# Performance work log

Hardware: AMD Instinct MI355X
Metric: run time of the kernel (lower is better)

Reference implementation:

```python
import jax, jax.numpy as jnp
import numpy as np

B, L, H, P, A, T = 64, 256, 1024, 64, 512, 8


def setup_inputs() -> dict:
    key = jax.random.key(0)
    ks = jax.random.split(key, 9)
    return {
        "word_hiddens": jax.random.normal(ks[0], (B, L, H), dtype=jnp.float32),
        "pos_e1_embeddings": jax.random.normal(ks[1], (B, L, P), dtype=jnp.float32),
        "pos_e2_embeddings": jax.random.normal(ks[2], (B, L, P), dtype=jnp.float32),
        "e1_end": jax.random.randint(ks[3], (B,), 0, L, dtype=jnp.int32),
        "e2_end": jax.random.randint(ks[4], (B,), 0, L, dtype=jnp.int32),
        "type_embeddings": jax.random.normal(ks[5], (T, H), dtype=jnp.float32) * 0.03,
        "W_pos": jax.random.normal(ks[6], (H + 2 * P, A), dtype=jnp.float32) * 0.03,
        "W_ent": jax.random.normal(ks[7], (4 * H, A), dtype=jnp.float32) * 0.02,
        "v": jax.random.normal(ks[8], (A,), dtype=jnp.float32) * 0.05,
    }


def _latent_type(e_h, type_emb):
    # alpha = softmax(e_h @ C^T); latent type = alpha @ C   (C: [T, latent])
    scores = jnp.einsum("bh,th->bt", e_h, type_emb)
    alpha = jax.nn.softmax(scores, axis=-1)
    return jnp.einsum("bt,th->bh", alpha, type_emb)


def reference(word_hiddens, pos_e1_embeddings, pos_e2_embeddings, e1_end, e2_end,
              type_embeddings, W_pos, W_ent, v):
    b, seq_len, h = word_hiddens.shape
    batch_idx = jnp.arange(b)
    e1_h = word_hiddens[batch_idx, e1_end]          # [B, H]
    e2_h = word_hiddens[batch_idx, e2_end]          # [B, H]
    e1_type = _latent_type(e1_h, type_embeddings)   # [B, H]
    e2_type = _latent_type(e2_h, type_embeddings)   # [B, H]

    entity_features = jnp.concatenate([e1_h, e1_type, e2_h, e2_type], axis=-1)  # [B, 4H]
    pos_features = jnp.concatenate([word_hiddens, pos_e1_embeddings, pos_e2_embeddings], axis=-1)  # [B, L, H+2P]

    dense_pos = jnp.einsum("blf,fa->bla", pos_features, W_pos)   # [B, L, A]
    dense_ent = entity_features @ W_ent                          # [B, A]
    # Faithful to original tf.repeat(axis=1)+reshape (element-interleaved, not a broadcast)
    dense_ent_r = jnp.repeat(dense_ent, seq_len, axis=1).reshape(b, seq_len, -1)  # [B, L, A]

    u = jnp.tanh(dense_pos + dense_ent_r)            # [B, L, A]
    vu = jnp.einsum("bla,a->bl", u, v)               # [B, L]
    alpha = jax.nn.softmax(vu, axis=-1)              # [B, L]
    z = jnp.einsum("blh,bl->bh", word_hiddens, alpha)  # [B, H]
    return z
```

## Files before the change

kernel.cpp:

```cpp
#include <hip/hip_runtime.h>
#include <hip/hip_bf16.h>
#include <math.h>

#define B_ 64
#define L_ 256
#define H_ 1024
#define P_ 64
#define A_ 512
#define T_ 8
#define KDIM 1152
#define NSTEP 36

typedef __attribute__((ext_vector_type(8))) __bf16 bf16x8;
typedef __attribute__((ext_vector_type(4))) float f32x4;

__device__ __forceinline__ float bf2f(ushort u) {
  union { unsigned int i; float f; } v; v.i = ((unsigned int)u) << 16; return v.f;
}
__device__ __forceinline__ ushort f2bf_rne(float f) {
  union { float f; unsigned int i; } v; v.f = f;
  unsigned int r = v.i + 0x7FFFu + ((v.i >> 16) & 1u);
  return (ushort)(r >> 16);
}
__device__ __forceinline__ unsigned int pack2_rne(float a, float b) {
  return (unsigned int)f2bf_rne(a) | ((unsigned int)f2bf_rne(b) << 16);
}

template <bool BF16>
__device__ __forceinline__ float ld1(const void* p, size_t i) {
  if (BF16) return bf2f(((const ushort*)p)[i]);
  return ((const float*)p)[i];
}
template <bool BF16>
__device__ __forceinline__ float4 ld4(const void* p, size_t i) {
  if (BF16) {
    ushort4 u = *(const ushort4*)((const ushort*)p + i);
    return (float4){bf2f(u.x), bf2f(u.y), bf2f(u.z), bf2f(u.w)};
  }
  return *(const float4*)((const float*)p + i);
}

__global__ __launch_bounds__(256) void detect_dtype(const ushort* __restrict__ wh,
                                                    int* __restrict__ flag) {
  __shared__ int cnt;
  if (threadIdx.x == 0) cnt = 0;
  __syncthreads();
  int c = 0;
  for (int i = threadIdx.x; i < 8192; i += 256) {
    int e = (wh[i] >> 7) & 0xFF;
    if (e >= 110 && e <= 135) c++;
  }
  atomicAdd(&cnt, c);
  __syncthreads();
  if (threadIdx.x == 0) flag[0] = (cnt > 6553) ? 1 : 0;
}

template <bool BF16>
__global__ __launch_bounds__(256) void build_wts(const void* __restrict__ W,
                                                 ushort* __restrict__ WTs,
                                                 const int* __restrict__ flag) {
  if ((*flag != 0) != BF16) return;
  __shared__ ushort tile[32][33];
  const int s  = blockIdx.x >> 4;
  const int at = blockIdx.x & 15;
  const int tx = threadIdx.x & 31;
  const int ty = threadIdx.x >> 5;
#pragma unroll
  for (int i = 0; i < 4; ++i) {
    size_t idx = (size_t)(s * 32 + ty + i * 8) * A_ + at * 32 + tx;
    ushort u;
    if (BF16) u = ((const ushort*)W)[idx];
    else u = f2bf_rne(((const float*)W)[idx]);
    tile[ty + i * 8][tx] = u;
  }
  __syncthreads();
#pragma unroll
  for (int i = 0; i < 4; ++i) {
    WTs[(size_t)s * (A_ * 32) + (size_t)(at * 32 + ty + i * 8) * 32 + tx] =
        tile[tx][ty + i * 8];
  }
}

template <bool BF16>
__global__ __launch_bounds__(256) void entity_features_k(
    const void* __restrict__ wh, const int* __restrict__ e1e,
    const int* __restrict__ e2e, const void* __restrict__ temb,
    float* __restrict__ EF, const int* __restrict__ flag) {
  if ((*flag != 0) != BF16) return;
  const int b = blockIdx.x;
  const int tid = threadIdx.x;
  __shared__ float eh1[1024];
  __shared__ float eh2[1024];
  __shared__ float part[256][16];
  __shared__ float scores[16];
  __shared__ float alpha[16];

  const size_t o1 = ((size_t)b * L_ + e1e[b]) * H_;
  const size_t o2 = ((size_t)b * L_ + e2e[b]) * H_;
  for (int h = tid; h < 1024; h += 256) {
    eh1[h] = ld1<BF16>(wh, o1 + h);
    eh2[h] = ld1<BF16>(wh, o2 + h);
  }
  __syncthreads();

  float p[16];
#pragma unroll
  for (int t = 0; t < 16; ++t) p[t] = 0.f;
  for (int h = tid; h < 1024; h += 256) {
    float a1 = eh1[h], a2 = eh2[h];
#pragma unroll
    for (int t = 0; t < 8; ++t) {
      float c = ld1<BF16>(temb, t * 1024 + h);
      p[t] += a1 * c;
      p[8 + t] += a2 * c;
    }
  }
#pragma unroll
  for (int t = 0; t < 16; ++t) part[tid][t] = p[t];
  __syncthreads();
  if (tid < 16) {
    float s = 0.f;
    for (int i = 0; i < 256; ++i) s += part[i][tid];
    scores[tid] = s;
  }
  __syncthreads();
  if (tid < 2) {
    const int base = tid * 8;
    float mx = scores[base];
    for (int t = 1; t < 8; ++t) mx = fmaxf(mx, scores[base + t]);
    float sum = 0.f;
    float e[8];
    for (int t = 0; t < 8; ++t) { e[t] = __expf(scores[base + t] - mx); sum += e[t]; }
    float inv = 1.f / sum;
    for (int t = 0; t < 8; ++t) alpha[base + t] = e[t] * inv;
  }
  __syncthreads();

  float* efb = EF + (size_t)b * 4096;
  for (int h = tid; h < 1024; h += 256) {
    float l1 = 0.f, l2 = 0.f;
#pragma unroll
    for (int t = 0; t < 8; ++t) {
      float c = ld1<BF16>(temb, t * 1024 + h);
      l1 += alpha[t] * c;
      l2 += alpha[8 + t] * c;
    }
    efb[h] = eh1[h];
    efb[1024 + h] = l1;
    efb[2048 + h] = eh2[h];
    efb[3072 + h] = l2;
  }
}

template <bool BF16>
__global__ __launch_bounds__(256) void ent_gemm(const float* __restrict__ EF,
                                                const void* __restrict__ went,
                                                float* __restrict__ part,
                                                const int* __restrict__ flag) {
  if ((*flag != 0) != BF16) return;
  const int nb = blockIdx.x & 3;
  const int kb = blockIdx.x >> 2;
  const int tid = threadIdx.x;
  __shared__ float efs[64][128];

  const int k0 = kb * 128;
  {
    const int kq = (tid & 31) * 4;
    for (int m = tid >> 5; m < 64; m += 8) {
      *(float4*)&efs[m][kq] = *(const float4*)&EF[(size_t)m * 4096 + k0 + kq];
    }
  }
  __syncthreads();

  const int n0 = nb * 128 + (tid & 31) * 4;
  const int mg = (tid >> 5) * 8;
  float acc[8][4];
#pragma unroll
  for (int i = 0; i < 8; ++i)
#pragma unroll
    for (int j = 0; j < 4; ++j) acc[i][j] = 0.f;

  for (int k = 0; k < 128; ++k) {
    float4 w = ld4<BF16>(went, (size_t)(k0 + k) * A_ + n0);
#pragma unroll
    for (int i = 0; i < 8; ++i) {
      float e = efs[mg + i][k];
      acc[i][0] += e * w.x;
      acc[i][1] += e * w.y;
      acc[i][2] += e * w.z;
      acc[i][3] += e * w.w;
    }
  }
#pragma unroll
  for (int i = 0; i < 8; ++i) {
    *(float4*)&part[((size_t)kb * 64 + mg + i) * A_ + n0] =
        (float4){acc[i][0], acc[i][1], acc[i][2], acc[i][3]};
  }
}

__global__ __launch_bounds__(256) void ent_reduce(const float* __restrict__ part,
                                                  float* __restrict__ dense_ent) {
  const int idx = blockIdx.x * 256 + threadIdx.x;
  float s = 0.f;
#pragma unroll
  for (int kb = 0; kb < 32; ++kb) s += part[(size_t)kb * 32768 + idx];
  dense_ent[idx] = s;
}

template <bool BF16>
__global__ __launch_bounds__(256) void fused_gemm_vu(
    const void* __restrict__ wh, const void* __restrict__ pe1,
    const void* __restrict__ pe2, const ushort* __restrict__ WTs,
    const float* __restrict__ dense_ent, const void* __restrict__ vvec,
    float* __restrict__ vu_part, const int* __restrict__ flag) {
  if ((*flag != 0) != BF16) return;
  __shared__ __align__(16) ushort Abuf[2][64 * 40];
  __shared__ __align__(16) ushort Bbuf[2][256 * 40];
  __shared__ float vu_s[4][64];

  const int tid = threadIdx.x;
  const int nb = blockIdx.x & 1;
  const int mb = blockIdx.x >> 1;
  const int rbase = mb * 64;
  const int wave = tid >> 6;
  const int lane = tid & 63;
  const int quad = lane >> 4;
  const int col = lane & 15;

  const int arow = tid >> 2;
  const int akq = (tid & 3) * 8;
  const int myrow = rbase + arow;
  const ushort* bbase = WTs + (size_t)nb * (256 * 32) + (size_t)tid * 32;

  f32x4 acc[4][4];
#pragma unroll
  for (int i = 0; i < 4; ++i)
#pragma unroll
    for (int j = 0; j < 4; ++j) acc[i][j] = (f32x4){0.f, 0.f, 0.f, 0.f};

  uint4 aR, bR0, bR1;

  {
    const size_t off = (size_t)myrow * H_ + 0 * 32 + akq;
    if (BF16) {
      aR = *(const uint4*)((const ushort*)wh + off);
    } else {
      float4 f0 = *(const float4*)((const float*)wh + off);
      float4 f1 = *(const float4*)((const float*)wh + off + 4);
      aR.x = pack2_rne(f0.x, f0.y); aR.y = pack2_rne(f0.z, f0.w);
      aR.z = pack2_rne(f1.x, f1.y); aR.w = pack2_rne(f1.z, f1.w);
    }
    const ushort* bs = bbase;
    bR0 = *(const uint4*)(bs + 0);
    bR1 = *(const uint4*)(bs + 8);
  }
  uint4 bR2 = *(const uint4*)(bbase + 16);
  uint4 bR3 = *(const uint4*)(bbase + 24);
  {
    *(uint4*)&Abuf[0][arow * 40 + akq] = aR;
    ushort* bd = &Bbuf[0][tid * 40];
    *(uint4*)(bd + 0)  = bR0;
    *(uint4*)(bd + 8)  = bR1;
    *(uint4*)(bd + 16) = bR2;
    *(uint4*)(bd + 24) = bR3;
  }
  __syncthreads();

  for (int s = 0; s < NSTEP; ++s) {
    const int cur = s & 1;

    if (s < NSTEP - 1) {
      const int sn = s + 1;
      const void* srcA;
      int ldA, k0A;
      if (sn < 32)      { srcA = wh;  ldA = H_; k0A = sn * 32; }
      else if (sn < 34) { srcA = pe1; ldA = P_; k0A = (sn - 32) * 32; }
      else              { srcA = pe2; ldA = P_; k0A = (sn - 34) * 32; }
      const size_t off = (size_t)myrow * ldA + k0A + akq;
      if (BF16) {
        aR = *(const uint4*)((const ushort*)srcA + off);
      } else {
        float4 f0 = *(const float4*)((const float*)srcA + off);
        float4 f1 = *(const float4*)((const float*)srcA + off + 4);
        aR.x = pack2_rne(f0.x, f0.y); aR.y = pack2_rne(f0.z, f0.w);
        aR.z = pack2_rne(f1.x, f1.y); aR.w = pack2_rne(f1.z, f1.w);
      }
      const ushort* bs = bbase + (size_t)sn * (A_ * 32);
      bR0 = *(const uint4*)(bs + 0);
      bR1 = *(const uint4*)(bs + 8);
      bR2 = *(const uint4*)(bs + 16);
      bR3 = *(const uint4*)(bs + 24);
    }

    bf16x8 af[4], bfr[4];
#pragma unroll
    for (int mf = 0; mf < 4; ++mf)
      af[mf] = *(const bf16x8*)&Abuf[cur][(mf * 16 + col) * 40 + quad * 8];
#pragma unroll
    for (int nf = 0; nf < 4; ++nf)
      bfr[nf] = *(const bf16x8*)&Bbuf[cur][(wave * 64 + nf * 16 + col) * 40 + quad * 8];
#pragma unroll
    for (int mf = 0; mf < 4; ++mf)
#pragma unroll
      for (int nf = 0; nf < 4; ++nf)
        acc[mf][nf] = __builtin_amdgcn_mfma_f32_16x16x32_bf16(af[mf], bfr[nf], acc[mf][nf], 0, 0, 0);

    if (s < NSTEP - 1) {
      const int nxt = cur ^ 1;
      *(uint4*)&Abuf[nxt][arow * 40 + akq] = aR;
      ushort* bd = &Bbuf[nxt][tid * 40];
      *(uint4*)(bd + 0)  = bR0;
      *(uint4*)(bd + 8)  = bR1;
      *(uint4*)(bd + 16) = bR2;
      *(uint4*)(bd + 24) = bR3;
      __syncthreads();
    }
  }

  float vv[4];
#pragma unroll
  for (int nf = 0; nf < 4; ++nf)
    vv[nf] = ld1<BF16>(vvec, nb * 256 + wave * 64 + nf * 16 + col);

#pragma unroll
  for (int mf = 0; mf < 4; ++mf) {
    const int row0 = mf * 16 + quad * 4;
    const int r0 = rbase + row0;
    const int bidx = r0 >> 8;
    const int l0 = r0 & 255;
    const float* ebase = dense_ent + bidx * A_ + 2 * l0 + nb;
    float e0 = ebase[0], e1 = ebase[2], e2 = ebase[4], e3 = ebase[6];
    float s0 = 0.f, s1 = 0.f, s2 = 0.f, s3 = 0.f;
#pragma unroll
    for (int nf = 0; nf < 4; ++nf) {
      float vn = vv[nf];
      s0 += tanhf(acc[mf][nf][0] + e0) * vn;
      s1 += tanhf(acc[mf][nf][1] + e1) * vn;
      s2 += tanhf(acc[mf][nf][2] + e2) * vn;
      s3 += tanhf(acc[mf][nf][3] + e3) * vn;
    }
    s0 += __shfl_xor(s0, 1); s0 += __shfl_xor(s0, 2); s0 += __shfl_xor(s0, 4); s0 += __shfl_xor(s0, 8);
    s1 += __shfl_xor(s1, 1); s1 += __shfl_xor(s1, 2); s1 += __shfl_xor(s1, 4); s1 += __shfl_xor(s1, 8);
    s2 += __shfl_xor(s2, 1); s2 += __shfl_xor(s2, 2); s2 += __shfl_xor(s2, 4); s2 += __shfl_xor(s2, 8);
    s3 += __shfl_xor(s3, 1); s3 += __shfl_xor(s3, 2); s3 += __shfl_xor(s3, 4); s3 += __shfl_xor(s3, 8);
    if (col == 0) {
      vu_s[wave][row0 + 0] = s0;
      vu_s[wave][row0 + 1] = s1;
      vu_s[wave][row0 + 2] = s2;
      vu_s[wave][row0 + 3] = s3;
    }
  }
  __syncthreads();
  if (tid < 64) {
    float s = vu_s[0][tid] + vu_s[1][tid] + vu_s[2][tid] + vu_s[3][tid];
    vu_part[(size_t)nb * (B_ * L_) + rbase + tid] = s;
  }
}

template <bool BF16>
__global__ __launch_bounds__(256) void softmax_z(const void* __restrict__ wh,
                                                 const float* __restrict__ vu_part,
                                                 void* __restrict__ out,
                                                 const int* __restrict__ flag) {
  if ((*flag != 0) != BF16) return;
  const int b = blockIdx.x >> 2;
  const int hq = blockIdx.x & 3;
  const int tid = threadIdx.x;
  __shared__ float alpha[256];
  __shared__ float red[256];

  float x = vu_part[b * L_ + tid] + vu_part[B_ * L_ + b * L_ + tid];
  red[tid] = x;
  __syncthreads();
  for (int s = 128; s > 0; s >>= 1) {
    if (tid < s) red[tid] = fmaxf(red[tid], red[tid + s]);
    __syncthreads();
  }
  float m = red[0];
  __syncthreads();
  float e = __expf(x - m);
  red[tid] = e;
  __syncthreads();
  for (int s = 128; s > 0; s >>= 1) {
    if (tid < s) red[tid] += red[tid + s];
    __syncthreads();
  }
  alpha[tid] = e / red[0];
  __syncthreads();

  const int h = hq * 256 + tid;
  const size_t base = (size_t)b * L_ * H_ + h;
  float a0 = 0.f, a1 = 0.f, a2 = 0.f, a3 = 0.f;
  for (int l = 0; l < 256; l += 4) {
    a0 += alpha[l + 0] * ld1<BF16>(wh, base + (size_t)(l + 0) * H_);
    a1 += alpha[l + 1] * ld1<BF16>(wh, base + (size_t)(l + 1) * H_);
    a2 += alpha[l + 2] * ld1<BF16>(wh, base + (size_t)(l + 2) * H_);
    a3 += alpha[l + 3] * ld1<BF16>(wh, base + (size_t)(l + 3) * H_);
  }
  float z = (a0 + a1) + (a2 + a3);
  if (BF16) ((ushort*)out)[b * H_ + h] = f2bf_rne(z);
  else ((float*)out)[b * H_ + h] = z;
}

extern "C" void kernel_launch(void* const* d_in, const int* in_sizes, int n_in,
                              void* d_out, int out_size, void* d_ws, size_t ws_size,
                              hipStream_t stream) {
  const void* wh   = d_in[0];
  const void* pe1  = d_in[1];
  const void* pe2  = d_in[2];
  const int*  e1e  = (const int*)d_in[3];
  const int*  e2e  = (const int*)d_in[4];
  const void* temb = d_in[5];
  const void* wpos = d_in[6];
  const void* went = d_in[7];
  const void* vvec = d_in[8];

  char* ws = (char*)d_ws;
  int*   flag      = (int*)ws;
  ushort* WTs      = (ushort*)(ws + 256);
  float* dense_ent = (float*)(ws + 1179904);
  float* vu_part   = (float*)(ws + 1310976);
  float* EF        = (float*)(ws + 1442048);
  float* part      = (float*)(ws + 2490624);

  detect_dtype<<<dim3(1), dim3(256), 0, stream>>>((const ushort*)wh, flag);

  build_wts<true ><<<dim3(576), dim3(256), 0, stream>>>(wpos, WTs, flag);
  build_wts<false><<<dim3(576), dim3(256), 0, stream>>>(wpos, WTs, flag);

  entity_features_k<true ><<<dim3(64), dim3(256), 0, stream>>>(wh, e1e, e2e, temb, EF, flag);
  entity_features_k<false><<<dim3(64), dim3(256), 0, stream>>>(wh, e1e, e2e, temb, EF, flag);

  ent_gemm<true ><<<dim3(128), dim3(256), 0, stream>>>(EF, went, part, flag);
  ent_gemm<false><<<dim3(128), dim3(256), 0, stream>>>(EF, went, part, flag);

  ent_reduce<<<dim3(128), dim3(256), 0, stream>>>(part, dense_ent);

  fused_gemm_vu<true ><<<dim3(512), dim3(256), 0, stream>>>(wh, pe1, pe2, WTs, dense_ent, vvec, vu_part, flag);
  fused_gemm_vu<false><<<dim3(512), dim3(256), 0, stream>>>(wh, pe1, pe2, WTs, dense_ent, vvec, vu_part, flag);

  softmax_z<true ><<<dim3(256), dim3(256), 0, stream>>>(wh, vu_part, d_out, flag);
  softmax_z<false><<<dim3(256), dim3(256), 0, stream>>>(wh, vu_part, d_out, flag);
}
```

Measured before the change: 217.1 us.

## Pick dtype on host, retile fused GEMM to 4 N-blocks, split entity GEMM

Removes the on-device dtype detection kernel and the paired bf16/fp32 launches guarded by a flag. The dtype is now chosen on the host from the input byte size, so only one launch runs per stage. The fused position GEMM now uses 128-column N tiles across 4 N-blocks with a 2x2 wave layout, giving 1024 blocks. The entity GEMM is split over M halves, giving 256 blocks. The softmax-weighted sum is unrolled to 8 accumulators, and the workspace is repacked so EF and vu_part share memory. This aims to cut launch overhead and improve occupancy, at the cost of extra B-tile reloads, more partial vu sums, and relying on in_sizes to infer the dtype.

```diff
diff --git a/kernel.cpp b/kernel.cpp
--- a/kernel.cpp
+++ b/kernel.cpp
@@ -40,26 +40,9 @@
   return *(const float4*)((const float*)p + i);
 }
 
-__global__ __launch_bounds__(256) void detect_dtype(const ushort* __restrict__ wh,
-                                                    int* __restrict__ flag) {
-  __shared__ int cnt;
-  if (threadIdx.x == 0) cnt = 0;
-  __syncthreads();
-  int c = 0;
-  for (int i = threadIdx.x; i < 8192; i += 256) {
-    int e = (wh[i] >> 7) & 0xFF;
-    if (e >= 110 && e <= 135) c++;
-  }
-  atomicAdd(&cnt, c);
-  __syncthreads();
-  if (threadIdx.x == 0) flag[0] = (cnt > 6553) ? 1 : 0;
-}
-
 template <bool BF16>
 __global__ __launch_bounds__(256) void build_wts(const void* __restrict__ W,
-                                                 ushort* __restrict__ WTs,
-                                                 const int* __restrict__ flag) {
-  if ((*flag != 0) != BF16) return;
+                                                 ushort* __restrict__ WTs) {
   __shared__ ushort tile[32][33];
   const int s  = blockIdx.x >> 4;
   const int at = blockIdx.x & 15;
@@ -85,8 +68,7 @@
 __global__ __launch_bounds__(256) void entity_features_k(
     const void* __restrict__ wh, const int* __restrict__ e1e,
     const int* __restrict__ e2e, const void* __restrict__ temb,
-    float* __restrict__ EF, const int* __restrict__ flag) {
-  if ((*flag != 0) != BF16) return;
+    float* __restrict__ EF) {
   const int b = blockIdx.x;
   const int tid = threadIdx.x;
   __shared__ float eh1[1024];
@@ -155,35 +137,34 @@
 template <bool BF16>
 __global__ __launch_bounds__(256) void ent_gemm(const float* __restrict__ EF,
                                                 const void* __restrict__ went,
-                                                float* __restrict__ part,
-                                                const int* __restrict__ flag) {
-  if ((*flag != 0) != BF16) return;
-  const int nb = blockIdx.x & 3;
-  const int kb = blockIdx.x >> 2;
+                                                float* __restrict__ part) {
+  const int mh = blockIdx.x & 1;
+  const int nb = (blockIdx.x >> 1) & 3;
+  const int kb = blockIdx.x >> 3;
   const int tid = threadIdx.x;
-  __shared__ float efs[64][128];
+  __shared__ float efs[32][128];
 
   const int k0 = kb * 128;
   {
     const int kq = (tid & 31) * 4;
-    for (int m = tid >> 5; m < 64; m += 8) {
-      *(float4*)&efs[m][kq] = *(const float4*)&EF[(size_t)m * 4096 + k0 + kq];
+    for (int m = tid >> 5; m < 32; m += 8) {
+      *(float4*)&efs[m][kq] = *(const float4*)&EF[(size_t)(mh * 32 + m) * 4096 + k0 + kq];
     }
   }
   __syncthreads();
 
   const int n0 = nb * 128 + (tid & 31) * 4;
-  const int mg = (tid >> 5) * 8;
-  float acc[8][4];
-#pragma unroll
-  for (int i = 0; i < 8; ++i)
+  const int mg = (tid >> 5) * 4;
+  float acc[4][4];
+#pragma unroll
+  for (int i = 0; i < 4; ++i)
 #pragma unroll
     for (int j = 0; j < 4; ++j) acc[i][j] = 0.f;
 
   for (int k = 0; k < 128; ++k) {
     float4 w = ld4<BF16>(went, (size_t)(k0 + k) * A_ + n0);
 #pragma unroll
-    for (int i = 0; i < 8; ++i) {
+    for (int i = 0; i < 4; ++i) {
       float e = efs[mg + i][k];
       acc[i][0] += e * w.x;
       acc[i][1] += e * w.y;
@@ -192,8 +173,8 @@
     }
   }
 #pragma unroll
-  for (int i = 0; i < 8; ++i) {
-    *(float4*)&part[((size_t)kb * 64 + mg + i) * A_ + n0] =
+  for (int i = 0; i < 4; ++i) {
+    *(float4*)&part[((size_t)kb * 64 + mh * 32 + mg + i) * A_ + n0] =
         (float4){acc[i][0], acc[i][1], acc[i][2], acc[i][3]};
   }
 }
@@ -212,36 +193,39 @@
     const void* __restrict__ wh, const void* __restrict__ pe1,
     const void* __restrict__ pe2, const ushort* __restrict__ WTs,
     const float* __restrict__ dense_ent, const void* __restrict__ vvec,
-    float* __restrict__ vu_part, const int* __restrict__ flag) {
-  if ((*flag != 0) != BF16) return;
+    float* __restrict__ vu_part) {
   __shared__ __align__(16) ushort Abuf[2][64 * 40];
-  __shared__ __align__(16) ushort Bbuf[2][256 * 40];
+  __shared__ __align__(16) ushort Bbuf[2][128 * 40];
   __shared__ float vu_s[4][64];
 
   const int tid = threadIdx.x;
-  const int nb = blockIdx.x & 1;
-  const int mb = blockIdx.x >> 1;
+  const int nb = blockIdx.x & 3;
+  const int mb = blockIdx.x >> 2;
   const int rbase = mb * 64;
   const int wave = tid >> 6;
   const int lane = tid & 63;
   const int quad = lane >> 4;
   const int col = lane & 15;
+  const int wr = wave >> 1;
+  const int wc = wave & 1;
 
   const int arow = tid >> 2;
   const int akq = (tid & 3) * 8;
   const int myrow = rbase + arow;
-  const ushort* bbase = WTs + (size_t)nb * (256 * 32) + (size_t)tid * 32;
-
-  f32x4 acc[4][4];
-#pragma unroll
-  for (int i = 0; i < 4; ++i)
+  const int brow = tid >> 1;
+  const int bk0 = (tid & 1) * 16;
+  const ushort* bbase = WTs + (size_t)(nb * 128 + brow) * 32 + bk0;
+
+  f32x4 acc[2][4];
+#pragma unroll
+  for (int i = 0; i < 2; ++i)
 #pragma unroll
     for (int j = 0; j < 4; ++j) acc[i][j] = (f32x4){0.f, 0.f, 0.f, 0.f};
 
   uint4 aR, bR0, bR1;
 
   {
-    const size_t off = (size_t)myrow * H_ + 0 * 32 + akq;
+    const size_t off = (size_t)myrow * H_ + akq;
     if (BF16) {
       aR = *(const uint4*)((const ushort*)wh + off);
     } else {
@@ -250,19 +234,14 @@
       aR.x = pack2_rne(f0.x, f0.y); aR.y = pack2_rne(f0.z, f0.w);
       aR.z = pack2_rne(f1.x, f1.y); aR.w = pack2_rne(f1.z, f1.w);
     }
-    const ushort* bs = bbase;
-    bR0 = *(const uint4*)(bs + 0);
-    bR1 = *(const uint4*)(bs + 8);
-  }
-  uint4 bR2 = *(const uint4*)(bbase + 16);
-  uint4 bR3 = *(const uint4*)(bbase + 24);
+    bR0 = *(const uint4*)(bbase + 0);
+    bR1 = *(const uint4*)(bbase + 8);
+  }
   {
     *(uint4*)&Abuf[0][arow * 40 + akq] = aR;
-    ushort* bd = &Bbuf[0][tid * 40];
-    *(uint4*)(bd + 0)  = bR0;
-    *(uint4*)(bd + 8)  = bR1;
-    *(uint4*)(bd + 16) = bR2;
-    *(uint4*)(bd + 24) = bR3;
+    ushort* bd = &Bbuf[0][brow * 40 + bk0];
+    *(uint4*)(bd + 0) = bR0;
+    *(uint4*)(bd + 8) = bR1;
   }
   __syncthreads();
 
@@ -288,19 +267,17 @@
       const ushort* bs = bbase + (size_t)sn * (A_ * 32);
       bR0 = *(const uint4*)(bs + 0);
       bR1 = *(const uint4*)(bs + 8);
-      bR2 = *(const uint4*)(bs + 16);
-      bR3 = *(const uint4*)(bs + 24);
-    }
-
-    bf16x8 af[4], bfr[4];
-#pragma unroll
-    for (int mf = 0; mf < 4; ++mf)
-      af[mf] = *(const bf16x8*)&Abuf[cur][(mf * 16 + col) * 40 + quad * 8];
+    }
+
+    bf16x8 af[2], bfr[4];
+#pragma unroll
+    for (int mf = 0; mf < 2; ++mf)
+      af[mf] = *(const bf16x8*)&Abuf[cur][(wr * 32 + mf * 16 + col) * 40 + quad * 8];
 #pragma unroll
     for (int nf = 0; nf < 4; ++nf)
-      bfr[nf] = *(const bf16x8*)&Bbuf[cur][(wave * 64 + nf * 16 + col) * 40 + quad * 8];
-#pragma unroll
-    for (int mf = 0; mf < 4; ++mf)
+      bfr[nf] = *(const bf16x8*)&Bbuf[cur][(wc * 64 + nf * 16 + col) * 40 + quad * 8];
+#pragma unroll
+    for (int mf = 0; mf < 2; ++mf)
 #pragma unroll
       for (int nf = 0; nf < 4; ++nf)
         acc[mf][nf] = __builtin_amdgcn_mfma_f32_16x16x32_bf16(af[mf], bfr[nf], acc[mf][nf], 0, 0, 0);
@@ -308,11 +285,9 @@
     if (s < NSTEP - 1) {
       const int nxt = cur ^ 1;
       *(uint4*)&Abuf[nxt][arow * 40 + akq] = aR;
-      ushort* bd = &Bbuf[nxt][tid * 40];
-      *(uint4*)(bd + 0)  = bR0;
-      *(uint4*)(bd + 8)  = bR1;
-      *(uint4*)(bd + 16) = bR2;
-      *(uint4*)(bd + 24) = bR3;
+      ushort* bd = &Bbuf[nxt][brow * 40 + bk0];
+      *(uint4*)(bd + 0) = bR0;
+      *(uint4*)(bd + 8) = bR1;
       __syncthreads();
     }
   }
@@ -320,15 +295,15 @@
   float vv[4];
 #pragma unroll
   for (int nf = 0; nf < 4; ++nf)
-    vv[nf] = ld1<BF16>(vvec, nb * 256 + wave * 64 + nf * 16 + col);
-
-#pragma unroll
-  for (int mf = 0; mf < 4; ++mf) {
-    const int row0 = mf * 16 + quad * 4;
+    vv[nf] = ld1<BF16>(vvec, nb * 128 + wc * 64 + nf * 16 + col);
+
+#pragma unroll
+  for (int mf = 0; mf < 2; ++mf) {
+    const int row0 = wr * 32 + mf * 16 + quad * 4;
     const int r0 = rbase + row0;
     const int bidx = r0 >> 8;
     const int l0 = r0 & 255;
-    const float* ebase = dense_ent + bidx * A_ + 2 * l0 + nb;
+    const float* ebase = dense_ent + bidx * A_ + 2 * l0 + (nb >> 1);
     float e0 = ebase[0], e1 = ebase[2], e2 = ebase[4], e3 = ebase[6];
     float s0 = 0.f, s1 = 0.f, s2 = 0.f, s3 = 0.f;
 #pragma unroll
@@ -352,7 +327,8 @@
   }
   __syncthreads();
   if (tid < 64) {
-    float s = vu_s[0][tid] + vu_s[1][tid] + vu_s[2][tid] + vu_s[3][tid];
+    const int wrr = tid >> 5;
+    float s = vu_s[wrr * 2][tid] + vu_s[wrr * 2 + 1][tid];
     vu_part[(size_t)nb * (B_ * L_) + rbase + tid] = s;
   }
 }
@@ -360,16 +336,16 @@
 template <bool BF16>
 __global__ __launch_bounds__(256) void softmax_z(const void* __restrict__ wh,
                                                  const float* __restrict__ vu_part,
-                                                 void* __restrict__ out,
-                                                 const int* __restrict__ flag) {
-  if ((*flag != 0) != BF16) return;
+                                                 void* __restrict__ out) {
   const int b = blockIdx.x >> 2;
   const int hq = blockIdx.x & 3;
   const int tid = threadIdx.x;
   __shared__ float alpha[256];
   __shared__ float red[256];
 
-  float x = vu_part[b * L_ + tid] + vu_part[B_ * L_ + b * L_ + tid];
+  float x = 0.f;
+#pragma unroll
+  for (int p = 0; p < 4; ++p) x += vu_part[(size_t)p * (B_ * L_) + b * L_ + tid];
   red[tid] = x;
   __syncthreads();
   for (int s = 128; s > 0; s >>= 1) {
@@ -391,13 +367,18 @@
   const int h = hq * 256 + tid;
   const size_t base = (size_t)b * L_ * H_ + h;
   float a0 = 0.f, a1 = 0.f, a2 = 0.f, a3 = 0.f;
-  for (int l = 0; l < 256; l += 4) {
+  float a4 = 0.f, a5 = 0.f, a6 = 0.f, a7 = 0.f;
+  for (int l = 0; l < 256; l += 8) {
     a0 += alpha[l + 0] * ld1<BF16>(wh, base + (size_t)(l + 0) * H_);
     a1 += alpha[l + 1] * ld1<BF16>(wh, base + (size_t)(l + 1) * H_);
     a2 += alpha[l + 2] * ld1<BF16>(wh, base + (size_t)(l + 2) * H_);
     a3 += alpha[l + 3] * ld1<BF16>(wh, base + (size_t)(l + 3) * H_);
-  }
-  float z = (a0 + a1) + (a2 + a3);
+    a4 += alpha[l + 4] * ld1<BF16>(wh, base + (size_t)(l + 4) * H_);
+    a5 += alpha[l + 5] * ld1<BF16>(wh, base + (size_t)(l + 5) * H_);
+    a6 += alpha[l + 6] * ld1<BF16>(wh, base + (size_t)(l + 6) * H_);
+    a7 += alpha[l + 7] * ld1<BF16>(wh, base + (size_t)(l + 7) * H_);
+  }
+  float z = ((a0 + a1) + (a2 + a3)) + ((a4 + a5) + (a6 + a7));
   if (BF16) ((ushort*)out)[b * H_ + h] = f2bf_rne(z);
   else ((float*)out)[b * H_ + h] = z;
 }
@@ -415,30 +396,28 @@
   const void* went = d_in[7];
   const void* vvec = d_in[8];
 
+  const bool bf16 = (in_sizes[0] == (int)(B_ * L_ * H_ * 2));
+
   char* ws = (char*)d_ws;
-  int*   flag      = (int*)ws;
-  ushort* WTs      = (ushort*)(ws + 256);
-  float* dense_ent = (float*)(ws + 1179904);
-  float* vu_part   = (float*)(ws + 1310976);
-  float* EF        = (float*)(ws + 1442048);
-  float* part      = (float*)(ws + 2490624);
-
-  detect_dtype<<<dim3(1), dim3(256), 0, stream>>>((const ushort*)wh, flag);
-
-  build_wts<true ><<<dim3(576), dim3(256), 0, stream>>>(wpos, WTs, flag);
-  build_wts<false><<<dim3(576), dim3(256), 0, stream>>>(wpos, WTs, flag);
-
-  entity_features_k<true ><<<dim3(64), dim3(256), 0, stream>>>(wh, e1e, e2e, temb, EF, flag);
-  entity_features_k<false><<<dim3(64), dim3(256), 0, stream>>>(wh, e1e, e2e, temb, EF, flag);
-
-  ent_gemm<true ><<<dim3(128), dim3(256), 0, stream>>>(EF, went, part, flag);
-  ent_gemm<false><<<dim3(128), dim3(256), 0, stream>>>(EF, went, part, flag);
-
-  ent_reduce<<<dim3(128), dim3(256), 0, stream>>>(part, dense_ent);
-
-  fused_gemm_vu<true ><<<dim3(512), dim3(256), 0, stream>>>(wh, pe1, pe2, WTs, dense_ent, vvec, vu_part, flag);
-  fused_gemm_vu<false><<<dim3(512), dim3(256), 0, stream>>>(wh, pe1, pe2, WTs, dense_ent, vvec, vu_part, flag);
-
-  softmax_z<true ><<<dim3(256), dim3(256), 0, stream>>>(wh, vu_part, d_out, flag);
-  softmax_z<false><<<dim3(256), dim3(256), 0, stream>>>(wh, vu_part, d_out, flag);
-}
+  ushort* WTs      = (ushort*)ws;
+  float* dense_ent = (float*)(ws + 1179648);
+  float* vu_part   = (float*)(ws + 1310720);
+  float* EF        = (float*)(ws + 1310720);
+  float* part      = (float*)(ws + 2359296);
+
+  if (bf16) {
+    build_wts<true ><<<dim3(576),  dim3(256), 0, stream>>>(wpos, WTs);
+    entity_features_k<true ><<<dim3(64), dim3(256), 0, stream>>>(wh, e1e, e2e, temb, EF);
+    ent_gemm<true ><<<dim3(256),  dim3(256), 0, stream>>>(EF, went, part);
+    ent_reduce<<<dim3(128), dim3(256), 0, stream>>>(part, dense_ent);
+    fused_gemm_vu<true ><<<dim3(1024), dim3(256), 0, stream>>>(wh, pe1, pe2, WTs, dense_ent, vvec, vu_part);
+    softmax_z<true ><<<dim3(256), dim3(256), 0, stream>>>(wh, vu_part, d_out);
+  } else {
+    build_wts<false><<<dim3(576),  dim3(256), 0, stream>>>(wpos, WTs);
+    entity_features_k<false><<<dim3(64), dim3(256), 0, stream>>>(wh, e1e, e2e, temb, EF);
+    ent_gemm<false><<<dim3(256),  dim3(256), 0, stream>>>(EF, went, part);
+    ent_reduce<<<dim3(128), dim3(256), 0, stream>>>(part, dense_ent);
+    fused_gemm_vu<false><<<dim3(1024), dim3(256), 0, stream>>>(wh, pe1, pe2, WTs, dense_ent, vvec, vu_part);
+    softmax_z<false><<<dim3(256), dim3(256), 0, stream>>>(wh, vu_part, d_out);
+  }
+}
```

Measured after the change: 192.9 us. 11.2% less time.
